# Kernel optimization log

Measured on AMD Instinct MI355X. Metric: run time of the kernel, lower is better.

## Reference

```python
import jax, jax.numpy as jnp
import numpy as np

NUM_EMBEDDINGS = 1024
EMBEDDING_DIM = 256

def setup_inputs() -> dict:
    key = jax.random.key(0)
    k1, k2 = jax.random.split(key)
    z_e = jax.random.normal(k1, (32, 256, 64, 64), dtype=jnp.float32)
    # nn.Embedding weight init uniform_(-1/K, 1/K)
    lim = 1.0 / NUM_EMBEDDINGS
    codebook = jax.random.uniform(k2, (NUM_EMBEDDINGS, EMBEDDING_DIM), dtype=jnp.float32,
                                  minval=-lim, maxval=lim)
    return {"z_e": z_e, "codebook": codebook}

def reference(z_e, codebook):
    B, C, H, W = z_e.shape
    # [B,C,H,W] -> [B*H*W, C]
    z_flat = jnp.transpose(z_e, (0, 2, 3, 1)).reshape(-1, C)
    # squared L2 distances: ||z||^2 + ||e||^2 - 2 z.e  -> [N, K]
    distances = (jnp.sum(z_flat ** 2, axis=1, keepdims=True)
                 + jnp.sum(codebook ** 2, axis=1)
                 - 2.0 * jnp.matmul(z_flat, codebook.T))
    encoding_indices = jnp.argmin(distances, axis=1)  # [N]
    z_q = codebook[encoding_indices].reshape(B, H, W, C)
    z_q = jnp.transpose(z_q, (0, 3, 1, 2))  # [B,C,H,W]
    sg = jax.lax.stop_gradient
    codebook_loss = jnp.mean((sg(z_q) - z_e) ** 2)
    commitment_loss = jnp.mean((sg(z_e) - z_q) ** 2)
    return z_q, codebook_loss + 0.25 * commitment_loss, encoding_indices
```

## Files before the change

kernel.cpp:

```cpp
#include <hip/hip_runtime.h>
#include <stdint.h>

typedef __attribute__((ext_vector_type(8))) _Float16 half8;
typedef __attribute__((ext_vector_type(4))) float f32x4;

#define CDIM 256
#define KCODES 1024
#define NPTS 131072
#define ZQ_ELEMS 33554432u
#define CAP 32768
#define MARGIN 3.0e-4f

#define WS_IMG 0
#define WS_S2 (16 * 65536)
#define WS_IDX (WS_S2 + 4096)
#define WS_PART (WS_IDX + NPTS * 4)
#define WS_CNT (WS_PART + 65536)
#define WS_LIST (WS_CNT + 64)

__device__ __forceinline__ float np_pairwise_sq_256(const float* x) {
    float res[2];
#pragma unroll
    for (int h = 0; h < 2; h++) {
        const float* a = x + h * 128;
        float r[8];
#pragma unroll
        for (int j = 0; j < 8; j++) r[j] = __fmul_rn(a[j], a[j]);
#pragma unroll
        for (int i = 8; i < 128; i += 8)
#pragma unroll
            for (int j = 0; j < 8; j++)
                r[j] = __fadd_rn(r[j], __fmul_rn(a[i + j], a[i + j]));
        res[h] = __fadd_rn(__fadd_rn(__fadd_rn(r[0], r[1]), __fadd_rn(r[2], r[3])),
                           __fadd_rn(__fadd_rn(r[4], r[5]), __fadd_rn(r[6], r[7])));
    }
    return __fadd_rn(res[0], res[1]);
}

__global__ __launch_bounds__(256) void vq_prep(const float* __restrict__ cb,
                                               unsigned char* __restrict__ img,
                                               int* __restrict__ cnt) {
    int t = threadIdx.x;
    if (blockIdx.x == 0 && t == 0) *cnt = 0;
    int codeLocal = t >> 5;
    int cg = t & 31;
    int k = blockIdx.x * 8 + codeLocal;
    const float* row = cb + k * CDIM + cg * 8;
    union H { _Float16 h[8]; uint4 u; } hi;
#pragma unroll
    for (int j = 0; j < 8; j++) hi.h[j] = (_Float16)(row[j] * 1024.f);
    int chunk = k >> 6, rowi = k & 63;
    int ks = cg >> 2, l4 = cg & 3;
    int cth = rowi >> 5, q = (rowi >> 4) & 1, l15 = rowi & 15;
    int lane = l4 * 16 + l15;
    *(uint4*)(img + chunk * 32768 + (((ks * 2 + cth) * 2 + q) << 10) + lane * 16) = hi.u;
}

__global__ __launch_bounds__(256) void vq_s2prep(const float* __restrict__ cb,
                                                 float* __restrict__ s2) {
    int k = blockIdx.x * 256 + threadIdx.x;
    float e[256];
#pragma unroll
    for (int c = 0; c < 256; c++) e[c] = cb[(size_t)k * CDIM + c];
    s2[k] = np_pairwise_sq_256(e);
}

__global__ __launch_bounds__(256, 2) void vq_dist(const float* __restrict__ z,
                                                  const unsigned char* __restrict__ img,
                                                  const float* __restrict__ s2g,
                                                  int* __restrict__ outIdx,
                                                  int* __restrict__ cnt,
                                                  int* __restrict__ list) {
    __shared__ __align__(16) unsigned char smem[2][32768];
    __shared__ float e2s[1024];
    int t = threadIdx.x;
    int lane = t & 63, wave = t >> 6;
    int l15 = lane & 15, l4 = lane >> 4;
    int blk0 = blockIdx.x * 128;
    int wbase = blk0 + wave * 32;
    int b = blk0 >> 12;
    int hwb0 = blk0 & 4095;
    const float* zb = z + (size_t)b * (CDIM * 4096);

#pragma unroll
    for (int i = 0; i < 8; i++) {
        size_t off = (size_t)(i * 256 + t) * 16;
        __builtin_amdgcn_global_load_lds(
            (const __attribute__((address_space(1))) void*)(img + off),
            (__attribute__((address_space(3))) void*)(&smem[0][0] + off), 16, 0, 0);
    }
#pragma unroll
    for (int i = 0; i < 4; i++) e2s[t + i * 256] = s2g[t + i * 256];

    half8 aHi[2][8], aLo[2][8];
#pragma unroll
    for (int ks = 0; ks < 8; ks++) {
        __syncthreads();
#pragma unroll
        for (int i = 0; i < 4; i++) {
            int u = i * 256 + t;
            int row = u >> 5, col4 = u & 31;
            const float* gsrc = zb + (size_t)(ks * 32 + row) * 4096 + hwb0 + col4 * 4;
            __builtin_amdgcn_global_load_lds(
                (const __attribute__((address_space(1))) void*)gsrc,
                (__attribute__((address_space(3))) void*)(&smem[1][0] + (size_t)u * 16), 16, 0, 0);
        }
        __syncthreads();
#pragma unroll
        for (int m = 0; m < 2; m++) {
            half8 h, l;
#pragma unroll
            for (int j = 0; j < 8; j++) {
                float f = *(const float*)(&smem[1][0] +
                        (size_t)(((l4 * 8 + j) * 128) + wave * 32 + m * 16 + l15) * 4) * 32.f;
                _Float16 fh = (_Float16)f;
                h[j] = fh;
                l[j] = (_Float16)(f - (float)fh);
            }
            aHi[m][ks] = h;
            aLo[m][ks] = l;
        }
    }
    __syncthreads();

    float bestv[2][4], bestv2[2][4];
    int besti[2][4];
#pragma unroll
    for (int m = 0; m < 2; m++)
#pragma unroll
        for (int j = 0; j < 4; j++) { bestv[m][j] = 3.0e38f; bestv2[m][j] = 3.0e38f; besti[m][j] = 0; }

    int cur = 0;
    for (int chunk = 0; chunk < 16; chunk++) {
        if (chunk < 15) {
            const unsigned char* src = img + (chunk + 1) * 32768;
            unsigned char* dst = &smem[cur ^ 1][0];
#pragma unroll
            for (int i = 0; i < 8; i++) {
                size_t off = (size_t)(i * 256 + t) * 16;
                __builtin_amdgcn_global_load_lds(
                    (const __attribute__((address_space(1))) void*)(src + off),
                    (__attribute__((address_space(3))) void*)(dst + off), 16, 0, 0);
            }
        }

        f32x4 accH[2][4], accL[2][4];
#pragma unroll
        for (int m = 0; m < 2; m++)
#pragma unroll
            for (int ct = 0; ct < 4; ct++) {
                accH[m][ct] = (f32x4){0.f, 0.f, 0.f, 0.f};
                accL[m][ct] = (f32x4){0.f, 0.f, 0.f, 0.f};
            }

        const unsigned char* bufc = &smem[cur][0];
#pragma unroll
        for (int ks = 0; ks < 8; ks++) {
#pragma unroll
            for (int cth = 0; cth < 2; cth++) {
                const unsigned char* fb = bufc + (((ks * 2 + cth) * 2) << 10) + lane * 16;
                half8 bh[2];
                bh[0] = *(const half8*)(fb);
                bh[1] = *(const half8*)(fb + 1024);
#pragma unroll
                for (int q = 0; q < 2; q++) {
                    int ct = cth * 2 + q;
#pragma unroll
                    for (int m = 0; m < 2; m++) {
                        accH[m][ct] = __builtin_amdgcn_mfma_f32_16x16x32_f16(aHi[m][ks], bh[q], accH[m][ct], 0, 0, 0);
                        accL[m][ct] = __builtin_amdgcn_mfma_f32_16x16x32_f16(aLo[m][ks], bh[q], accL[m][ct], 0, 0, 0);
                    }
                }
            }
        }
#pragma unroll
        for (int ct = 0; ct < 4; ct++) {
            int code = chunk * 64 + ct * 16 + l15;
            float ev = e2s[code];
#pragma unroll
            for (int m = 0; m < 2; m++)
#pragma unroll
                for (int j = 0; j < 4; j++) {
                    float a = accH[m][ct][j] + accL[m][ct][j];
                    float s = fmaf(a, -6.103515625e-05f, ev);
                    if (s < bestv[m][j]) { bestv2[m][j] = bestv[m][j]; bestv[m][j] = s; besti[m][j] = code; }
                    else if (s < bestv2[m][j]) bestv2[m][j] = s;
                }
        }
        __syncthreads();
        cur ^= 1;
    }

#pragma unroll
    for (int m = 0; m < 2; m++)
#pragma unroll
        for (int j = 0; j < 4; j++) {
            float v = bestv[m][j], v2 = bestv2[m][j];
            int idx = besti[m][j];
#pragma unroll
            for (int off = 1; off < 16; off <<= 1) {
                float ov = __shfl_xor(v, off);
                float ov2 = __shfl_xor(v2, off);
                int oi = __shfl_xor(idx, off);
                if (ov < v || (ov == v && oi < idx)) { v2 = fminf(v, ov2); v = ov; idx = oi; }
                else v2 = fminf(v2, ov);
            }
            if (l15 == 0) {
                int p = wbase + m * 16 + l4 * 4 + j;
                outIdx[p] = idx;
                if (v2 - v < MARGIN) {
                    int pos = atomicAdd(cnt, 1);
                    if (pos < CAP) list[pos] = p;
                }
            }
        }
}

__global__ __launch_bounds__(256) void vq_cbt(const float* __restrict__ cb,
                                              float* __restrict__ cbT) {
    int k = blockIdx.x * 256 + threadIdx.x;
    for (int c = 0; c < 256; c++) cbT[c * 1024 + k] = cb[(size_t)k * 256 + c];
}

__global__ __launch_bounds__(256) void vq_rescue(const float* __restrict__ z,
                                                 const float* __restrict__ cbT,
                                                 const float* __restrict__ s2,
                                                 const int* __restrict__ list,
                                                 const int* __restrict__ cnt,
                                                 int* __restrict__ outIdx) {
    __shared__ float zs[8][256];
    __shared__ float S1s[8];
    __shared__ float rv[256];
    __shared__ int ri[256];
    int n = *cnt; if (n > CAP) n = CAP;
    int t = threadIdx.x;
    for (int base = blockIdx.x * 8; base < n; base += gridDim.x * 8) {
        int npts = n - base; if (npts > 8) npts = 8;
        __syncthreads();
        {
            int pp = t >> 5, c0 = (t & 31) * 8;
            if (pp < npts) {
                int p = list[base + pp];
                int b = p >> 12, hw = p & 4095;
                const float* zp = z + ((size_t)b << 20) + hw;
#pragma unroll
                for (int j = 0; j < 8; j++) zs[pp][c0 + j] = zp[(size_t)(c0 + j) << 12];
            }
        }
        __syncthreads();
        if (t < npts) S1s[t] = np_pairwise_sq_256(zs[t]);
        __syncthreads();

        float d[8][4];
#pragma unroll
        for (int pp = 0; pp < 8; pp++)
#pragma unroll
            for (int q = 0; q < 4; q++) d[pp][q] = 0.f;
        for (int c = 0; c < 256; c++) {
            const float* er = cbT + c * 1024 + t;
            float e0 = er[0], e1 = er[256], e2v = er[512], e3 = er[768];
#pragma unroll
            for (int pp = 0; pp < 8; pp++) {
                float zc = zs[pp][c];
                d[pp][0] = fmaf(zc, e0, d[pp][0]);
                d[pp][1] = fmaf(zc, e1, d[pp][1]);
                d[pp][2] = fmaf(zc, e2v, d[pp][2]);
                d[pp][3] = fmaf(zc, e3, d[pp][3]);
            }
        }
        float s2v[4] = {s2[t], s2[256 + t], s2[512 + t], s2[768 + t]};

        float bv[8]; int bi[8];
#pragma unroll
        for (int pp = 0; pp < 8; pp++) {
            float v = 3.4e38f; int i0 = 0;
#pragma unroll
            for (int q = 0; q < 4; q++) {
                float dist = __fsub_rn(__fadd_rn(S1s[pp], s2v[q]), __fmul_rn(2.0f, d[pp][q]));
                if (dist < v) { v = dist; i0 = q * 256 + t; }
            }
            bv[pp] = v; bi[pp] = i0;
        }
        for (int pp = 0; pp < 8; pp++) {
            if (pp >= npts) break;
            rv[t] = bv[pp]; ri[t] = bi[pp];
            __syncthreads();
            for (int sft = 128; sft > 0; sft >>= 1) {
                if (t < sft) {
                    if (rv[t + sft] < rv[t] || (rv[t + sft] == rv[t] && ri[t + sft] < ri[t])) {
                        rv[t] = rv[t + sft]; ri[t] = ri[t + sft];
                    }
                }
                __syncthreads();
            }
            if (t == 0) outIdx[list[base + pp]] = ri[0];
            __syncthreads();
        }
    }
}

__global__ __launch_bounds__(256) void vq_gather(const float* __restrict__ z,
                                                 const float* __restrict__ cb,
                                                 const int* __restrict__ idxs,
                                                 float* __restrict__ out,
                                                 float* __restrict__ partial) {
    int tid = blockIdx.x * 256 + threadIdx.x;
    int hw = tid & 4095;
    int bg = tid >> 12;
    int b = bg >> 5, cg = bg & 31;
    int id = idxs[(b << 12) + hw];
    const float4* cr = (const float4*)(cb + (size_t)id * CDIM + cg * 8);
    float4 v0 = cr[0], v1 = cr[1];
    float va[8] = {v0.x, v0.y, v0.z, v0.w, v1.x, v1.y, v1.z, v1.w};
    size_t base = ((size_t)(b * 256 + cg * 8) << 12) + hw;
    float s = 0.f;
#pragma unroll
    for (int j = 0; j < 8; j++) {
        float ze = z[base + ((size_t)j << 12)];
        out[base + ((size_t)j << 12)] = va[j];
        float d = va[j] - ze;
        s = fmaf(d, d, s);
    }
    if (cg == 0) out[(size_t)ZQ_ELEMS + 1u + (b << 12) + hw] = (float)id;
#pragma unroll
    for (int off = 32; off > 0; off >>= 1) s += __shfl_down(s, off);
    __shared__ float red[4];
    if ((threadIdx.x & 63) == 0) red[threadIdx.x >> 6] = s;
    __syncthreads();
    if (threadIdx.x == 0) partial[blockIdx.x] = red[0] + red[1] + red[2] + red[3];
}

__global__ __launch_bounds__(512) void vq_finalize(const float* __restrict__ partial,
                                                   float* __restrict__ out) {
    int t = threadIdx.x;
    double s = 0.0;
    for (int i = t; i < 16384; i += 512) s += (double)partial[i];
#pragma unroll
    for (int off = 32; off > 0; off >>= 1) s += __shfl_down(s, off);
    __shared__ double sd[8];
    if ((t & 63) == 0) sd[t >> 6] = s;
    __syncthreads();
    if (t == 0) {
        double tot = sd[0] + sd[1] + sd[2] + sd[3] + sd[4] + sd[5] + sd[6] + sd[7];
        out[ZQ_ELEMS] = (float)(1.25 * tot / (double)ZQ_ELEMS);
    }
}

extern "C" void kernel_launch(void* const* d_in, const int* in_sizes, int n_in,
                              void* d_out, int out_size, void* d_ws, size_t ws_size,
                              hipStream_t stream) {
    const float* z = (const float*)d_in[0];
    const float* cb = (const float*)d_in[1];
    unsigned char* ws = (unsigned char*)d_ws;
    unsigned char* img = ws + WS_IMG;
    float* cbT = (float*)(ws + WS_IMG);
    float* s2 = (float*)(ws + WS_S2);
    int* idx = (int*)(ws + WS_IDX);
    float* partial = (float*)(ws + WS_PART);
    int* cnt = (int*)(ws + WS_CNT);
    int* list = (int*)(ws + WS_LIST);
    float* out = (float*)d_out;

    vq_prep<<<128, 256, 0, stream>>>(cb, img, cnt);
    vq_s2prep<<<4, 256, 0, stream>>>(cb, s2);
    vq_dist<<<1024, 256, 0, stream>>>(z, img, s2, idx, cnt, list);
    vq_cbt<<<4, 256, 0, stream>>>(cb, cbT);
    vq_rescue<<<512, 256, 0, stream>>>(z, cbT, s2, list, cnt, idx);
    vq_gather<<<16384, 256, 0, stream>>>(z, cb, idx, out, partial);
    vq_finalize<<<1, 512, 0, stream>>>(partial, out);
}
```

Baseline: 383.9 us.

## Read codebook fragments directly from global memory instead of LDS double buffer

Removes the double-buffered LDS staging of the pre-swizzled fp16 codebook image and has each wave load its B fragments straight from global memory (L2/L1 cached), dropping the per-chunk barriers. LDS use falls from 64KB to 16KB, which could allow more blocks per CU and removes synchronisation. The trade-off is that each wave now issues its own global loads with no explicit prefetch, so MFMA work may stall on global/L2 latency.

Result: slower. 442.9 us (+15.4%).

```diff
diff --git a/kernel.cpp b/kernel.cpp
--- a/kernel.cpp
+++ b/kernel.cpp
@@ -71,7 +71,7 @@
                                                   int* __restrict__ outIdx,
                                                   int* __restrict__ cnt,
                                                   int* __restrict__ list) {
-    __shared__ __align__(16) unsigned char smem[2][32768];
+    __shared__ __align__(16) unsigned char az[16384];
     __shared__ float e2s[1024];
     int t = threadIdx.x;
     int lane = t & 63, wave = t >> 6;
@@ -83,13 +83,6 @@
     const float* zb = z + (size_t)b * (CDIM * 4096);
 
 #pragma unroll
-    for (int i = 0; i < 8; i++) {
-        size_t off = (size_t)(i * 256 + t) * 16;
-        __builtin_amdgcn_global_load_lds(
-            (const __attribute__((address_space(1))) void*)(img + off),
-            (__attribute__((address_space(3))) void*)(&smem[0][0] + off), 16, 0, 0);
-    }
-#pragma unroll
     for (int i = 0; i < 4; i++) e2s[t + i * 256] = s2g[t + i * 256];
 
     half8 aHi[2][8], aLo[2][8];
@@ -103,7 +96,7 @@
             const float* gsrc = zb + (size_t)(ks * 32 + row) * 4096 + hwb0 + col4 * 4;
             __builtin_amdgcn_global_load_lds(
                 (const __attribute__((address_space(1))) void*)gsrc,
-                (__attribute__((address_space(3))) void*)(&smem[1][0] + (size_t)u * 16), 16, 0, 0);
+                (__attribute__((address_space(3))) void*)(az + (size_t)u * 16), 16, 0, 0);
         }
         __syncthreads();
 #pragma unroll
@@ -111,7 +104,7 @@
             half8 h, l;
 #pragma unroll
             for (int j = 0; j < 8; j++) {
-                float f = *(const float*)(&smem[1][0] +
+                float f = *(const float*)(az +
                         (size_t)(((l4 * 8 + j) * 128) + wave * 32 + m * 16 + l15) * 4) * 32.f;
                 _Float16 fh = (_Float16)f;
                 h[j] = fh;
@@ -121,7 +114,6 @@
             aLo[m][ks] = l;
         }
     }
-    __syncthreads();
 
     float bestv[2][4], bestv2[2][4];
     int besti[2][4];
@@ -130,19 +122,9 @@
 #pragma unroll
         for (int j = 0; j < 4; j++) { bestv[m][j] = 3.0e38f; bestv2[m][j] = 3.0e38f; besti[m][j] = 0; }
 
-    int cur = 0;
+    const unsigned char* cbase0 = img + (size_t)lane * 16;
     for (int chunk = 0; chunk < 16; chunk++) {
-        if (chunk < 15) {
-            const unsigned char* src = img + (chunk + 1) * 32768;
-            unsigned char* dst = &smem[cur ^ 1][0];
-#pragma unroll
-            for (int i = 0; i < 8; i++) {
-                size_t off = (size_t)(i * 256 + t) * 16;
-                __builtin_amdgcn_global_load_lds(
-                    (const __attribute__((address_space(1))) void*)(src + off),
-                    (__attribute__((address_space(3))) void*)(dst + off), 16, 0, 0);
-            }
-        }
+        const unsigned char* cbase = cbase0 + (size_t)chunk * 32768;
 
         f32x4 accH[2][4], accL[2][4];
 #pragma unroll
@@ -153,23 +135,20 @@
                 accL[m][ct] = (f32x4){0.f, 0.f, 0.f, 0.f};
             }
 
-        const unsigned char* bufc = &smem[cur][0];
 #pragma unroll
         for (int ks = 0; ks < 8; ks++) {
 #pragma unroll
             for (int cth = 0; cth < 2; cth++) {
-                const unsigned char* fb = bufc + (((ks * 2 + cth) * 2) << 10) + lane * 16;
-                half8 bh[2];
-                bh[0] = *(const half8*)(fb);
-                bh[1] = *(const half8*)(fb + 1024);
-#pragma unroll
-                for (int q = 0; q < 2; q++) {
-                    int ct = cth * 2 + q;
-#pragma unroll
-                    for (int m = 0; m < 2; m++) {
-                        accH[m][ct] = __builtin_amdgcn_mfma_f32_16x16x32_f16(aHi[m][ks], bh[q], accH[m][ct], 0, 0, 0);
-                        accL[m][ct] = __builtin_amdgcn_mfma_f32_16x16x32_f16(aLo[m][ks], bh[q], accL[m][ct], 0, 0, 0);
-                    }
+                const unsigned char* fb = cbase + (((ks * 2 + cth) * 2) << 10);
+                half8 bh0 = *(const half8*)(fb);
+                half8 bh1 = *(const half8*)(fb + 1024);
+#pragma unroll
+                for (int m = 0; m < 2; m++) {
+                    int ct0 = cth * 2;
+                    accH[m][ct0] = __builtin_amdgcn_mfma_f32_16x16x32_f16(aHi[m][ks], bh0, accH[m][ct0], 0, 0, 0);
+                    accL[m][ct0] = __builtin_amdgcn_mfma_f32_16x16x32_f16(aLo[m][ks], bh0, accL[m][ct0], 0, 0, 0);
+                    accH[m][ct0 + 1] = __builtin_amdgcn_mfma_f32_16x16x32_f16(aHi[m][ks], bh1, accH[m][ct0 + 1], 0, 0, 0);
+                    accL[m][ct0 + 1] = __builtin_amdgcn_mfma_f32_16x16x32_f16(aLo[m][ks], bh1, accL[m][ct0 + 1], 0, 0, 0);
                 }
             }
         }
@@ -187,8 +166,6 @@
                     else if (s < bestv2[m][j]) bestv2[m][j] = s;
                 }
         }
-        __syncthreads();
-        cur ^= 1;
     }
 
 #pragma unroll
```

## Drop low-half fp16 compensation for z and shrink codebook chunks to 32 codes

Applied to the files above, without the earlier changes.

The distance kernel no longer splits z into high and low fp16 parts. This removes the second (compensation) MFMA stream and its accumulators, halving matrix work and register pressure. Codebook chunks drop from 64 to 32 codes, which halves shared memory per buffer, and the launch bound is raised to three blocks per CU for higher occupancy. The cost is lower dot-product precision: near-tie candidates may now exceed the fixed refinement margin, so the chosen index could differ from the reference.

After: 372.2 us. 3.0% less time.

```diff
diff --git a/kernel.cpp b/kernel.cpp
--- a/kernel.cpp
+++ b/kernel.cpp
@@ -49,11 +49,11 @@
     union H { _Float16 h[8]; uint4 u; } hi;
 #pragma unroll
     for (int j = 0; j < 8; j++) hi.h[j] = (_Float16)(row[j] * 1024.f);
-    int chunk = k >> 6, rowi = k & 63;
+    int chunk = k >> 5, rowi = k & 31;
     int ks = cg >> 2, l4 = cg & 3;
-    int cth = rowi >> 5, q = (rowi >> 4) & 1, l15 = rowi & 15;
+    int q = rowi >> 4, l15 = rowi & 15;
     int lane = l4 * 16 + l15;
-    *(uint4*)(img + chunk * 32768 + (((ks * 2 + cth) * 2 + q) << 10) + lane * 16) = hi.u;
+    *(uint4*)(img + chunk * 16384 + ((ks * 2 + q) << 10) + lane * 16) = hi.u;
 }
 
 __global__ __launch_bounds__(256) void vq_s2prep(const float* __restrict__ cb,
@@ -65,13 +65,13 @@
     s2[k] = np_pairwise_sq_256(e);
 }
 
-__global__ __launch_bounds__(256, 2) void vq_dist(const float* __restrict__ z,
+__global__ __launch_bounds__(256, 3) void vq_dist(const float* __restrict__ z,
                                                   const unsigned char* __restrict__ img,
                                                   const float* __restrict__ s2g,
                                                   int* __restrict__ outIdx,
                                                   int* __restrict__ cnt,
                                                   int* __restrict__ list) {
-    __shared__ __align__(16) unsigned char smem[2][32768];
+    __shared__ __align__(16) unsigned char smem[2][16384];
     __shared__ float e2s[1024];
     int t = threadIdx.x;
     int lane = t & 63, wave = t >> 6;
@@ -83,7 +83,7 @@
     const float* zb = z + (size_t)b * (CDIM * 4096);
 
 #pragma unroll
-    for (int i = 0; i < 8; i++) {
+    for (int i = 0; i < 4; i++) {
         size_t off = (size_t)(i * 256 + t) * 16;
         __builtin_amdgcn_global_load_lds(
             (const __attribute__((address_space(1))) void*)(img + off),
@@ -92,7 +92,7 @@
 #pragma unroll
     for (int i = 0; i < 4; i++) e2s[t + i * 256] = s2g[t + i * 256];
 
-    half8 aHi[2][8], aLo[2][8];
+    half8 aHi[2][8];
 #pragma unroll
     for (int ks = 0; ks < 8; ks++) {
         __syncthreads();
@@ -108,17 +108,14 @@
         __syncthreads();
 #pragma unroll
         for (int m = 0; m < 2; m++) {
-            half8 h, l;
+            half8 h;
 #pragma unroll
             for (int j = 0; j < 8; j++) {
                 float f = *(const float*)(&smem[1][0] +
                         (size_t)(((l4 * 8 + j) * 128) + wave * 32 + m * 16 + l15) * 4) * 32.f;
-                _Float16 fh = (_Float16)f;
-                h[j] = fh;
-                l[j] = (_Float16)(f - (float)fh);
+                h[j] = (_Float16)f;
             }
             aHi[m][ks] = h;
-            aLo[m][ks] = l;
         }
     }
     __syncthreads();
@@ -131,12 +128,12 @@
         for (int j = 0; j < 4; j++) { bestv[m][j] = 3.0e38f; bestv2[m][j] = 3.0e38f; besti[m][j] = 0; }
 
     int cur = 0;
-    for (int chunk = 0; chunk < 16; chunk++) {
-        if (chunk < 15) {
-            const unsigned char* src = img + (chunk + 1) * 32768;
+    for (int chunk = 0; chunk < 32; chunk++) {
+        if (chunk < 31) {
+            const unsigned char* src = img + (size_t)(chunk + 1) * 16384;
             unsigned char* dst = &smem[cur ^ 1][0];
 #pragma unroll
-            for (int i = 0; i < 8; i++) {
+            for (int i = 0; i < 4; i++) {
                 size_t off = (size_t)(i * 256 + t) * 16;
                 __builtin_amdgcn_global_load_lds(
                     (const __attribute__((address_space(1))) void*)(src + off),
@@ -144,45 +141,32 @@
             }
         }
 
-        f32x4 accH[2][4], accL[2][4];
+        f32x4 acc[2][2];
 #pragma unroll
         for (int m = 0; m < 2; m++)
 #pragma unroll
-            for (int ct = 0; ct < 4; ct++) {
-                accH[m][ct] = (f32x4){0.f, 0.f, 0.f, 0.f};
-                accL[m][ct] = (f32x4){0.f, 0.f, 0.f, 0.f};
-            }
-
-        const unsigned char* bufc = &smem[cur][0];
+            for (int q = 0; q < 2; q++) acc[m][q] = (f32x4){0.f, 0.f, 0.f, 0.f};
+
+        const unsigned char* bufc = &smem[cur][0] + lane * 16;
 #pragma unroll
         for (int ks = 0; ks < 8; ks++) {
-#pragma unroll
-            for (int cth = 0; cth < 2; cth++) {
-                const unsigned char* fb = bufc + (((ks * 2 + cth) * 2) << 10) + lane * 16;
-                half8 bh[2];
-                bh[0] = *(const half8*)(fb);
-                bh[1] = *(const half8*)(fb + 1024);
-#pragma unroll
-                for (int q = 0; q < 2; q++) {
-                    int ct = cth * 2 + q;
-#pragma unroll
-                    for (int m = 0; m < 2; m++) {
-                        accH[m][ct] = __builtin_amdgcn_mfma_f32_16x16x32_f16(aHi[m][ks], bh[q], accH[m][ct], 0, 0, 0);
-                        accL[m][ct] = __builtin_amdgcn_mfma_f32_16x16x32_f16(aLo[m][ks], bh[q], accL[m][ct], 0, 0, 0);
-                    }
-                }
-            }
-        }
-#pragma unroll
-        for (int ct = 0; ct < 4; ct++) {
-            int code = chunk * 64 + ct * 16 + l15;
+            half8 b0 = *(const half8*)(bufc + (ks << 11));
+            half8 b1 = *(const half8*)(bufc + (ks << 11) + 1024);
+#pragma unroll
+            for (int m = 0; m < 2; m++) {
+                acc[m][0] = __builtin_amdgcn_mfma_f32_16x16x32_f16(aHi[m][ks], b0, acc[m][0], 0, 0, 0);
+                acc[m][1] = __builtin_amdgcn_mfma_f32_16x16x32_f16(aHi[m][ks], b1, acc[m][1], 0, 0, 0);
+            }
+        }
+#pragma unroll
+        for (int q = 0; q < 2; q++) {
+            int code = chunk * 32 + q * 16 + l15;
             float ev = e2s[code];
 #pragma unroll
             for (int m = 0; m < 2; m++)
 #pragma unroll
                 for (int j = 0; j < 4; j++) {
-                    float a = accH[m][ct][j] + accL[m][ct][j];
-                    float s = fmaf(a, -6.103515625e-05f, ev);
+                    float s = fmaf(acc[m][q][j], -6.103515625e-05f, ev);
                     if (s < bestv[m][j]) { bestv2[m][j] = bestv[m][j]; bestv[m][j] = s; besti[m][j] = code; }
                     else if (s < bestv2[m][j]) bestv2[m][j] = s;
                 }
```
